# Kernel tuning notes

Hardware: AMD Instinct MI355X
Metric: run time of the kernel (lower is better)

The kernel has to match this reference:

```python
import jax, jax.numpy as jnp
import numpy as np

T, D, TR, CC, L = 4096, 512, 64, 64, 3  # time, input_size, trace, context, num_blocks


def setup_inputs() -> dict:
    key = jax.random.key(0)
    ks = jax.random.split(key, 10)
    x = jax.random.normal(ks[0], (T, D), dtype=jnp.float32)
    state = jnp.zeros((L, 1, TR, CC), dtype=jnp.float32)  # initial recurrent state (real part; imag is 0)
    start = jax.random.uniform(ks[1], (T,)) < 0.02  # episode-reset mask
    Wtr = jax.random.normal(ks[2], (L, TR, D), dtype=jnp.float32) / np.float32(np.sqrt(D))
    Wc = jax.random.normal(ks[3], (L, TR, D), dtype=jnp.float32) / np.float32(np.sqrt(D))
    a = jax.random.uniform(ks[4], (L, TR), minval=1e-6, maxval=0.1)
    b = 2 * jnp.pi / jnp.exp(jax.random.uniform(ks[5], (L, CC), minval=0.0, maxval=float(np.log(10000.0))))
    F = 2 * TR * CC
    W0 = jax.random.normal(ks[6], (L, D, F), dtype=jnp.float32) * np.float32(0.01 / np.sqrt(F))  # default_init scale=0.01
    b0 = jnp.zeros((L, D)); g0 = jnp.ones((L, D)); beta0 = jnp.zeros((L, D))
    W1 = jax.random.normal(ks[7], (L, D, D), dtype=jnp.float32) / np.float32(np.sqrt(D))
    b1 = jnp.zeros((L, D)); g1 = jnp.ones((L, D)); beta1 = jnp.zeros((L, D))
    return dict(x=x, state=state, start=start, Wtr=Wtr, Wc=Wc, a=a, b=b,
                W0=W0, b0=b0, g0=g0, beta0=beta0, W1=W1, b1=b1, g1=g1, beta1=beta1)


def _layernorm(z, g, b):
    m = jnp.mean(z, axis=-1, keepdims=True)
    v = jnp.mean((z - m) ** 2, axis=-1, keepdims=True)
    return (z - m) / jnp.sqrt(v + 1e-5) * g + b


def _sffm(x, st0, start, Wtr, Wc, a, b, W0, b0, g0, bb0, W1, b1, g1, bb1):
    t_len = x.shape[0]
    tr = x @ Wtr.T           # [T, TR]
    ct = x @ Wc.T            # [T, CC] (context proj also has trace_size outputs)
    pre = jnp.abs(tr[:, :, None] * ct[:, None, :])            # [T, TR, CC]
    pre = pre / (1e-8 + jnp.sum(pre, axis=(-2, -1), keepdims=True))
    # complex decay per (trace, context) pair: exp((-|a| + i b) * dt)
    ab = (-jnp.abs(a))[:, None] + 1j * b[None, :]             # [TR, CC] complex64

    def combine(carry, inc):
        ps, s, i = carry
        st, xx, j = inc
        s = s * jnp.logical_not(st)                            # reset gating
        dt = (j - i).astype(jnp.float32)[:, None, None]
        new = s * jnp.exp(ab[None] * dt) + xx
        return (jnp.logical_or(st, ps), new, j)

    ts = jnp.arange(t_len + 1, dtype=jnp.int32)
    sb = jnp.concatenate([jnp.zeros((1, 1, 1), bool), start.reshape(t_len, 1, 1)], axis=0)
    xs = jnp.concatenate([st0.astype(jnp.complex64), pre.astype(jnp.complex64)], axis=0)
    _, ns, _ = jax.lax.associative_scan(combine, (sb, xs, ts), axis=0)
    ns = ns[1:]                                                # [T, TR, CC] complex

    s = ns.reshape(t_len, TR * CC)
    mag = jnp.log1p(jnp.abs(s))
    ang = jnp.angle(s)
    scaled = jnp.concatenate([mag * jnp.sin(ang), mag * jnp.cos(ang)], axis=-1)  # [T, 2*TR*CC]
    z = jax.nn.leaky_relu(_layernorm(scaled @ W0.T + b0, g0, bb0))
    z = jax.nn.leaky_relu(_layernorm(z @ W1.T + b1, g1, bb1))
    return z


def reference(x, state, start, Wtr, Wc, a, b, W0, b0, g0, beta0, W1, b1, g1, beta1):
    z = x
    for l in range(L):
        z = _sffm(x, state[l], start, Wtr[l], Wc[l], a[l], b[l],
                  W0[l], b0[l], g0[l], beta0[l], W1[l], b1[l], g1[l], beta1[l])
        x = x + z
    return z  # NSFFM returns the last block's y
```

## Files before the change

### kernel.cpp

```cpp
#include <hip/hip_runtime.h>
#include <hip/hip_bf16.h>
#include <math.h>

#define T_LEN 4096
#define D_DIM 512
#define F_DIM 8192
#define NCHUNK 64
#define CLEN 64

typedef short short8 __attribute__((ext_vector_type(8)));
typedef float f32x4 __attribute__((ext_vector_type(4)));
typedef unsigned short u16;
typedef unsigned int u32;

__device__ inline float wave_sum(float v) {
#pragma unroll
  for (int o = 32; o; o >>= 1) v += __shfl_xor(v, o);
  return v;
}

__device__ inline u16 f2bf_bits(float v) {
  __hip_bfloat16 h = __float2bfloat16(v);
  return *(u16*)&h;
}

__device__ inline float bf2f(u16 u) {
  u32 x = ((u32)u) << 16;
  return *(float*)&x;
}

__device__ inline void gl_lds16(const void* g, void* l) {
  __builtin_amdgcn_global_load_lds((const __attribute__((address_space(1))) void*)g,
                                   (__attribute__((address_space(3))) void*)l, 16, 0, 0);
}

__global__ void detect_start(const unsigned char* __restrict__ s8, int* __restrict__ mode) {
  __shared__ int found;
  if (threadIdx.x == 0) found = 0;
  __syncthreads();
  for (int i = threadIdx.x; i < 4096; i += 256)
    if ((i & 3) && s8[i]) found = 1;
  __syncthreads();
  if (threadIdx.x == 0) mode[0] = found;
}

__device__ inline int read_start(const unsigned char* s8, const int* s32, int mode, int t) {
  return mode ? (int)s8[t] : s32[t];
}

__global__ void f2bf(const float* __restrict__ s, u16* __restrict__ d, int n) {
  int i = blockIdx.x * 256 + threadIdx.x;
  if (i < n) d[i] = f2bf_bits(s[i]);
}

__global__ void k_conv(const float* __restrict__ wtr, const float* __restrict__ wc,
                       u16* __restrict__ wcat, const float* __restrict__ w0,
                       u16* __restrict__ w0bf) {
  int i = blockIdx.x * 256 + threadIdx.x;
  if (i < 128 * D_DIM) {
    float v = (i < 64 * D_DIM) ? wtr[i] : wc[i - 64 * D_DIM];
    wcat[i] = f2bf_bits(v);
  }
  int j = i - 128 * D_DIM;
  if (j >= 0 && j < D_DIM * F_DIM) {
    int d = j >> 13, f = j & 8191;
    int r = f >> 7, rem = f & 127;
    int c = rem >> 1, b = rem & 1;
    float v = w0[(size_t)d * 8192 + b * 4096 + r * 64 + c];
    w0bf[(size_t)d * 8192 + (f ^ ((d & 7) << 3))] = f2bf_bits(v);
  }
}

template <int BM, int BN, int WR, int WC>
__global__ __launch_bounds__(256) void gemm_bt(const u16* __restrict__ A,
                                               const u16* __restrict__ B,
                                               float* __restrict__ C, int M, int N, int K) {
  constexpr int BK = 32;
  constexpr int MT = BM / (WR * 16);
  constexpr int NT = BN / (WC * 16);
  constexpr int AG = BM / 64;
  constexpr int BG = BN / 64;
  __shared__ u16 sA[BM * BK];
  __shared__ u16 sB[BN * BK];
  const int m0 = blockIdx.x * BM;
  const int n0 = blockIdx.y * BN;
  const int tid = threadIdx.x;
  const int wave = tid >> 6;
  const int lane = tid & 63;
  const int wr = wave / WC;
  const int wc = wave % WC;
  const int row_l = tid >> 2;
  const int c8 = (tid & 3) << 3;
  const int frow = lane & 15;
  const int fcol = (lane >> 4) << 3;

  f32x4 acc[MT][NT];
#pragma unroll
  for (int i = 0; i < MT; ++i)
#pragma unroll
    for (int j = 0; j < NT; ++j) acc[i][j] = (f32x4){0.f, 0.f, 0.f, 0.f};

  for (int k0 = 0; k0 < K; k0 += BK) {
#pragma unroll
    for (int j = 0; j < AG; ++j) {
      uint4 v = *(const uint4*)(A + (size_t)(m0 + j * 64 + row_l) * K + (k0 + c8));
      *(uint4*)(sA + (j * 64 + row_l) * BK + c8) = v;
    }
#pragma unroll
    for (int j = 0; j < BG; ++j) {
      uint4 v = *(const uint4*)(B + (size_t)(n0 + j * 64 + row_l) * K + (k0 + c8));
      *(uint4*)(sB + (j * 64 + row_l) * BK + c8) = v;
    }
    __syncthreads();
    short8 af[MT], bfr[NT];
#pragma unroll
    for (int i = 0; i < MT; ++i)
      af[i] = *(const short8*)(sA + (wr * MT * 16 + i * 16 + frow) * BK + fcol);
#pragma unroll
    for (int j = 0; j < NT; ++j)
      bfr[j] = *(const short8*)(sB + (wc * NT * 16 + j * 16 + frow) * BK + fcol);
#pragma unroll
    for (int i = 0; i < MT; ++i)
#pragma unroll
      for (int j = 0; j < NT; ++j)
        acc[i][j] = __builtin_amdgcn_mfma_f32_16x16x32_bf16(af[i], bfr[j], acc[i][j], 0, 0, 0);
    __syncthreads();
  }
#pragma unroll
  for (int i = 0; i < MT; ++i) {
    const int rbase = m0 + wr * MT * 16 + i * 16 + ((lane >> 4) << 2);
#pragma unroll
    for (int j = 0; j < NT; ++j) {
      const int col = n0 + wc * NT * 16 + j * 16 + (lane & 15);
#pragma unroll
      for (int rg = 0; rg < 4; ++rg) C[(size_t)(rbase + rg) * N + col] = acc[i][j][rg];
    }
  }
}

__global__ __launch_bounds__(256) void gemm128(const u16* __restrict__ A,
                                               const u16* __restrict__ B,
                                               u16* __restrict__ Cp, size_t pstride, int N,
                                               int Ktot) {
  __shared__ u16 sA[128 * 64];
  __shared__ u16 sB[128 * 64];
  const int tid = threadIdx.x;
  const int wave = tid >> 6;
  const int lane = tid & 63;
  const int wr = wave >> 1;
  const int wc = wave & 1;
  const int m0 = blockIdx.x * 128;
  const int n0 = blockIdx.y * 128;
  const int ks = blockIdx.z;
  const int Kper = Ktot / gridDim.z;
  const int kb = ks * Kper;
  const int row_s = tid >> 3;
  const int g8 = (tid & 7) << 3;
  const int frow = lane & 15;
  const int quad = lane >> 4;
  const int sw = frow & 7;

  f32x4 acc[4][4];
#pragma unroll
  for (int i = 0; i < 4; ++i)
#pragma unroll
    for (int j = 0; j < 4; ++j) acc[i][j] = (f32x4){0.f, 0.f, 0.f, 0.f};

  for (int k0 = kb; k0 < kb + Kper; k0 += 64) {
#pragma unroll
    for (int j = 0; j < 4; ++j) {
      gl_lds16(A + (size_t)(m0 + j * 32 + row_s) * Ktot + (k0 + g8), sA + j * 2048 + wave * 512);
      gl_lds16(B + (size_t)(n0 + j * 32 + row_s) * Ktot + (k0 + g8), sB + j * 2048 + wave * 512);
    }
    asm volatile("s_waitcnt vmcnt(0)" ::: "memory");
    __syncthreads();
#pragma unroll
    for (int kk = 0; kk < 2; ++kk) {
      const int gA = (((kk << 2) | quad) ^ sw) << 3;
      short8 af[4], bfr[4];
#pragma unroll
      for (int i = 0; i < 4; ++i)
        af[i] = *(const short8*)(sA + (wr * 64 + i * 16 + frow) * 64 + gA);
#pragma unroll
      for (int j = 0; j < 4; ++j)
        bfr[j] = *(const short8*)(sB + (wc * 64 + j * 16 + frow) * 64 + gA);
#pragma unroll
      for (int i = 0; i < 4; ++i)
#pragma unroll
        for (int j = 0; j < 4; ++j)
          acc[i][j] = __builtin_amdgcn_mfma_f32_16x16x32_bf16(af[i], bfr[j], acc[i][j], 0, 0, 0);
    }
    __syncthreads();
  }
#pragma unroll
  for (int i = 0; i < 4; ++i) {
    const int rbase = m0 + wr * 64 + i * 16 + ((lane >> 4) << 2);
#pragma unroll
    for (int j = 0; j < 4; ++j) {
      const int col = n0 + wc * 64 + j * 16 + (lane & 15);
#pragma unroll
      for (int rg = 0; rg < 4; ++rg)
        Cp[(size_t)ks * pstride + (size_t)(rbase + rg) * N + col] = f2bf_bits(acc[i][j][rg]);
    }
  }
}

__global__ __launch_bounds__(512, 2) void gemm_8ph(const u16* __restrict__ A,
                                                   const u16* __restrict__ B,
                                                   u16* __restrict__ Cp, size_t pstride, int N,
                                                   int Ktot) {
  extern __shared__ u16 smem[];
  u16* sA = smem;
  u16* sB = smem + 32768;
  const int tid = threadIdx.x;
  const int wave = tid >> 6;
  const int lane = tid & 63;
  const int wr = wave >> 1;
  const int wc = wave & 1;
  const int m0 = blockIdx.x * 256;
  const int n0 = blockIdx.y * 128;
  const int ks = blockIdx.z;
  const int Kper = Ktot / gridDim.z;
  const int kb = ks * Kper;
  const int NITER = Kper >> 7;
  const int r_l = tid >> 3;
  const int g8 = (tid & 7) << 3;
  const int frow = lane & 15;
  const int quad = lane >> 4;
  const int sw = frow & 7;

  const u16* Abase = A + (size_t)(m0 + r_l) * Ktot + g8;
  const u16* Bbase = B + (size_t)(n0 + r_l) * Ktot + g8;

#define STAGE_A(l, k0, b) \
  gl_lds16(Abase + (size_t)(l) * 64 * Ktot + (k0), sA + (b)*16384 + (l)*4096 + wave * 512)
#define STAGE_B(l, k0, b) \
  gl_lds16(Bbase + (size_t)(l) * 64 * Ktot + (k0), sB + (b)*8192 + (l)*4096 + wave * 512)

  f32x4 acc[4][4];
#pragma unroll
  for (int i = 0; i < 4; ++i)
#pragma unroll
    for (int j = 0; j < 4; ++j) acc[i][j] = (f32x4){0.f, 0.f, 0.f, 0.f};

  STAGE_A(0, kb, 0);
  STAGE_A(1, kb, 0);
  STAGE_A(2, kb, 0);
  STAGE_A(3, kb, 0);
  STAGE_B(0, kb, 0);
  STAGE_B(1, kb, 0);
  STAGE_A(0, kb + 64, 1);
  STAGE_A(2, kb + 64, 1);
  asm volatile("s_waitcnt vmcnt(2)" ::: "memory");
  __builtin_amdgcn_s_barrier();

  short8 afr[2][2];
  short8 bf0[2][2];
  short8 bf1[2][2];

  for (int I = 0; I < NITER; ++I) {
    const int k0e = kb + (I << 7);
    const bool nl = (I < NITER - 1);
#pragma unroll
    for (int p = 0; p < 8; ++p) {
      const int b = p >> 2;
      const int q = p & 3;
      const int qm = q >> 1;
      const int qn = qm ^ (q & 1);
      if (q == 0 || q == 2) {
#pragma unroll
        for (int f = 0; f < 2; ++f)
#pragma unroll
          for (int kk = 0; kk < 2; ++kk)
            afr[f][kk] = *(const short8*)(sA + b * 16384 +
                                          (wr * 64 + (qm * 2 + f) * 16 + frow) * 64 +
                                          ((((kk << 2) | quad) ^ sw) << 3));
      }
      if (q == 0) {
#pragma unroll
        for (int g = 0; g < 2; ++g)
#pragma unroll
          for (int kk = 0; kk < 2; ++kk)
            bf0[g][kk] = *(const short8*)(sB + b * 8192 + (wc * 64 + g * 16 + frow) * 64 +
                                          ((((kk << 2) | quad) ^ sw) << 3));
      }
      if (q == 1) {
#pragma unroll
        for (int g = 0; g < 2; ++g)
#pragma unroll
          for (int kk = 0; kk < 2; ++kk)
            bf1[g][kk] = *(const short8*)(sB + b * 8192 + (wc * 64 + 32 + g * 16 + frow) * 64 +
                                          ((((kk << 2) | quad) ^ sw) << 3));
      }
      if (p == 0) { STAGE_A(1, k0e + 64, 1); STAGE_A(3, k0e + 64, 1); }
      if (p == 1) { STAGE_B(0, k0e + 64, 1); STAGE_B(1, k0e + 64, 1); }
      if (p == 3 && nl) { STAGE_A(0, k0e + 128, 0); STAGE_A(2, k0e + 128, 0); }
      if (p == 4 && nl) { STAGE_A(1, k0e + 128, 0); STAGE_A(3, k0e + 128, 0); }
      if (p == 5 && nl) { STAGE_B(0, k0e + 128, 0); STAGE_B(1, k0e + 128, 0); }
      if (p == 7 && nl) { STAGE_A(0, k0e + 192, 1); STAGE_A(2, k0e + 192, 1); }
      __builtin_amdgcn_s_barrier();
      asm volatile("s_waitcnt lgkmcnt(0)" ::: "memory");
      __builtin_amdgcn_sched_barrier(0);
      __builtin_amdgcn_s_setprio(1);
      if (qn == 0) {
#pragma unroll
        for (int f = 0; f < 2; ++f)
#pragma unroll
          for (int g = 0; g < 2; ++g)
#pragma unroll
            for (int kk = 0; kk < 2; ++kk)
              acc[qm * 2 + f][g] = __builtin_amdgcn_mfma_f32_16x16x32_bf16(
                  afr[f][kk], bf0[g][kk], acc[qm * 2 + f][g], 0, 0, 0);
      } else {
#pragma unroll
        for (int f = 0; f < 2; ++f)
#pragma unroll
          for (int g = 0; g < 2; ++g)
#pragma unroll
            for (int kk = 0; kk < 2; ++kk)
              acc[qm * 2 + f][2 + g] = __builtin_amdgcn_mfma_f32_16x16x32_bf16(
                  afr[f][kk], bf1[g][kk], acc[qm * 2 + f][2 + g], 0, 0, 0);
      }
      __builtin_amdgcn_s_setprio(0);
      if (p == 3) {
        if (nl)
          asm volatile("s_waitcnt vmcnt(2)" ::: "memory");
        else
          asm volatile("s_waitcnt vmcnt(0)" ::: "memory");
      }
      if (p == 7 && nl) asm volatile("s_waitcnt vmcnt(2)" ::: "memory");
      __builtin_amdgcn_s_barrier();
    }
  }
#undef STAGE_A
#undef STAGE_B

#pragma unroll
  for (int i = 0; i < 4; ++i) {
    const int rbase = m0 + wr * 64 + i * 16 + (quad << 2);
#pragma unroll
    for (int j = 0; j < 4; ++j) {
      const int col = n0 + wc * 64 + j * 16 + frow;
#pragma unroll
      for (int rg = 0; rg < 4; ++rg)
        Cp[(size_t)ks * pstride + (size_t)(rbase + rg) * N + col] = f2bf_bits(acc[i][j][rg]);
    }
  }
}

__global__ void prep_pq(const float* __restrict__ trct, float* __restrict__ pT,
                        float* __restrict__ q) {
  int t = blockIdx.x;
  int lane = threadIdx.x;
  float tr = trct[t * 128 + lane];
  float ct = trct[t * 128 + 64 + lane];
  float ap = fabsf(tr), aq = fabsf(ct);
  float Sp = wave_sum(ap);
  float Sq = wave_sum(aq);
  float denom = 1e-8f + Sp * Sq;
  pT[lane * T_LEN + t] = ap;
  q[t * 64 + lane] = aq / denom;
}

__global__ void scan_phase1(const float* __restrict__ pT, const float* __restrict__ q,
                            const unsigned char* __restrict__ st8, const int* __restrict__ st32,
                            const int* __restrict__ modep, const float* __restrict__ a,
                            const float* __restrict__ b, float4* __restrict__ chunkbuf) {
  int chunk = blockIdx.x, r = blockIdx.y, c = threadIdx.x;
  int mode = modep[0];
  int t0 = chunk * CLEN;
  float na = -fabsf(a[r]);
  float rho = __expf(na);
  float bb = b[c];
  float er = rho * __cosf(bb), ei = rho * __sinf(bb);
  float pv = pT[r * T_LEN + t0 + c];
  int sv = read_start(st8, st32, mode, t0 + c);
  unsigned long long bal = __ballot(sv != 0);
  float Ar, Ai;
  if (bal) {
    Ar = 0.f; Ai = 0.f;
  } else {
    float mag = __expf(64.f * na);
    float ang = 64.f * bb;
    Ar = mag * __cosf(ang);
    Ai = mag * __sinf(ang);
  }
  int L = bal ? (63 - __builtin_clzll(bal)) : 0;
  float Br = 0.f, Bi = 0.f;
  const float* qrow = q + (size_t)t0 * 64 + c;
  for (int i = L; i < CLEN; ++i) {
    float pre = __shfl(pv, i) * qrow[i * 64];
    float nBr = er * Br - ei * Bi + pre;
    Bi = er * Bi + ei * Br;
    Br = nBr;
  }
  chunkbuf[((size_t)chunk * 64 + r) * 64 + c] = make_float4(Ar, Ai, Br, Bi);
}

__global__ void scan_phase2(const float4* __restrict__ chunkbuf, const float* __restrict__ state,
                            float2* __restrict__ s0buf) {
  int r = blockIdx.x, c = threadIdx.x;
  float Sr = state[r * 64 + c], Si = 0.f;
  for (int k = 0; k < NCHUNK; ++k) {
    s0buf[((size_t)k * 64 + r) * 64 + c] = make_float2(Sr, Si);
    float4 ab = chunkbuf[((size_t)k * 64 + r) * 64 + c];
    float nSr = ab.x * Sr - ab.y * Si + ab.z;
    Si = ab.x * Si + ab.y * Sr + ab.w;
    Sr = nSr;
  }
}

__global__ void scan_phase3(const float* __restrict__ pT, const float* __restrict__ q,
                            const unsigned char* __restrict__ st8, const int* __restrict__ st32,
                            const int* __restrict__ modep, const float* __restrict__ a,
                            const float* __restrict__ b, const float2* __restrict__ s0buf,
                            u32* __restrict__ scaled, int c0) {
  int chunk = c0 + blockIdx.x, r = blockIdx.y, c = threadIdx.x;
  int mode = modep[0];
  int t0 = chunk * CLEN;
  float rho = __expf(-fabsf(a[r]));
  float bb = b[c];
  float er = rho * __cosf(bb), ei = rho * __sinf(bb);
  float pv = pT[r * T_LEN + t0 + c];
  int sv = read_start(st8, st32, mode, t0 + c);
  float2 s0 = s0buf[((size_t)chunk * 64 + r) * 64 + c];
  float Sr = s0.x, Si = s0.y;
  int tl0 = (chunk - c0) * CLEN;
  const float* qrow = q + (size_t)t0 * 64 + c;
  u32* srow = scaled + (size_t)tl0 * 4096;
  const int Ldw = r * 64 + c;
#pragma unroll 4
  for (int i = 0; i < CLEN; ++i) {
    float qt = qrow[i * 64];
    float pt = __shfl(pv, i);
    int st = __shfl(sv, i);
    float pre = pt * qt;
    float cer = st ? 0.f : er;
    float cei = st ? 0.f : ei;
    float nSr = cer * Sr - cei * Si + pre;
    Si = cer * Si + cei * Sr;
    Sr = nSr;
    float m2 = fmaf(Sr, Sr, Si * Si);
    float rsq = rsqrtf(fmaxf(m2, 1e-30f));
    float m = m2 * rsq;
    float sc = __log2f(1.0f + m) * 0.6931471805599453f * rsq;
    u32 pack = ((u32)f2bf_bits(sc * Sr) << 16) | (u32)f2bf_bits(sc * Si);
    srow[(size_t)i * 4096 + (Ldw ^ ((i & 7) << 2))] = pack;
  }
}

__global__ void ln_act16(const u16* __restrict__ parts, int KS, size_t pstride,
                         const float* __restrict__ bias, const float* __restrict__ gam,
                         const float* __restrict__ bet, u16* __restrict__ zbf) {
  __shared__ float red[8];
  int t = blockIdx.x, tid = threadIdx.x;
  size_t o = (size_t)t * D_DIM + tid;
  float v0 = bias[tid];
  float v1 = bias[tid + 256];
  for (int ks = 0; ks < KS; ++ks) {
    v0 += bf2f(parts[(size_t)ks * pstride + o]);
    v1 += bf2f(parts[(size_t)ks * pstride + o + 256]);
  }
  float s = wave_sum(v0 + v1);
  if ((tid & 63) == 0) red[tid >> 6] = s;
  __syncthreads();
  float mean = (red[0] + red[1] + red[2] + red[3]) * (1.f / 512.f);
  float d0 = v0 - mean, d1 = v1 - mean;
  float s2 = wave_sum(d0 * d0 + d1 * d1);
  if ((tid & 63) == 0) red[4 + (tid >> 6)] = s2;
  __syncthreads();
  float var = (red[4] + red[5] + red[6] + red[7]) * (1.f / 512.f);
  float rstd = rsqrtf(var + 1e-5f);
  float z0 = d0 * rstd * gam[tid] + bet[tid];
  float z1 = d1 * rstd * gam[tid + 256] + bet[tid + 256];
  z0 = z0 > 0.f ? z0 : 0.01f * z0;
  z1 = z1 > 0.f ? z1 : 0.01f * z1;
  zbf[o] = f2bf_bits(z0);
  zbf[o + 256] = f2bf_bits(z1);
}

__global__ void ln_act32(const float* __restrict__ y, const float* __restrict__ bias,
                         const float* __restrict__ gam, const float* __restrict__ bet,
                         const float* __restrict__ xsrc, float* __restrict__ xdst,
                         u16* __restrict__ xbf_next, float* __restrict__ finout) {
  __shared__ float red[8];
  int t = blockIdx.x, tid = threadIdx.x;
  size_t o = (size_t)t * D_DIM + tid;
  float v0 = y[o] + bias[tid];
  float v1 = y[o + 256] + bias[tid + 256];
  float s = wave_sum(v0 + v1);
  if ((tid & 63) == 0) red[tid >> 6] = s;
  __syncthreads();
  float mean = (red[0] + red[1] + red[2] + red[3]) * (1.f / 512.f);
  float d0 = v0 - mean, d1 = v1 - mean;
  float s2 = wave_sum(d0 * d0 + d1 * d1);
  if ((tid & 63) == 0) red[4 + (tid >> 6)] = s2;
  __syncthreads();
  float var = (red[4] + red[5] + red[6] + red[7]) * (1.f / 512.f);
  float rstd = rsqrtf(var + 1e-5f);
  float z0 = d0 * rstd * gam[tid] + bet[tid];
  float z1 = d1 * rstd * gam[tid + 256] + bet[tid + 256];
  z0 = z0 > 0.f ? z0 : 0.01f * z0;
  z1 = z1 > 0.f ? z1 : 0.01f * z1;
  if (xdst) {
    float x0 = xsrc[o] + z0, x1 = xsrc[o + 256] + z1;
    xdst[o] = x0;
    xdst[o + 256] = x1;
    xbf_next[o] = f2bf_bits(x0);
    xbf_next[o + 256] = f2bf_bits(x1);
  }
  if (finout) {
    finout[o] = z0;
    finout[o + 256] = z1;
  }
}

__global__ void err_signal(float* __restrict__ out, float code) {
  if (threadIdx.x == 0) out[0] = code;
}

extern "C" void kernel_launch(void* const* d_in, const int* in_sizes, int n_in, void* d_out,
                              int out_size, void* d_ws, size_t ws_size, hipStream_t stream) {
  const float* x_in = (const float*)d_in[0];
  const float* state = (const float*)d_in[1];
  const unsigned char* start8 = (const unsigned char*)d_in[2];
  const int* start32 = (const int*)d_in[2];
  const float* Wtr = (const float*)d_in[3];
  const float* Wc = (const float*)d_in[4];
  const float* a_in = (const float*)d_in[5];
  const float* b_in = (const float*)d_in[6];
  const float* W0 = (const float*)d_in[7];
  const float* b0 = (const float*)d_in[8];
  const float* g0 = (const float*)d_in[9];
  const float* beta0 = (const float*)d_in[10];
  const float* W1 = (const float*)d_in[11];
  const float* b1 = (const float*)d_in[12];
  const float* g1 = (const float*)d_in[13];
  const float* beta1 = (const float*)d_in[14];
  float* out = (float*)d_out;

  static int attr_state = 0;
  if (attr_state == 0)
    attr_state = (hipFuncSetAttribute((const void*)gemm_8ph,
                                      hipFuncAttributeMaxDynamicSharedMemorySize,
                                      98304) == hipSuccess)
                     ? 1
                     : -1;
  const bool attr_ok = (attr_state == 1);

  char* w = (char*)d_ws;
  auto alloc = [&](size_t bytes) {
    char* ptr = w;
    w += (bytes + 255) & ~(size_t)255;
    return ptr;
  };
  float* x_ws = (float*)alloc(4ull * T_LEN * D_DIM);
  u16* xbf = (u16*)alloc(2ull * T_LEN * D_DIM);
  u16* wcat = (u16*)alloc(2ull * 128 * D_DIM);
  u16* w0bf = (u16*)alloc(2ull * D_DIM * F_DIM);
  u16* w1bf = (u16*)alloc(2ull * 3 * D_DIM * D_DIM);
  float* trct = (float*)alloc(4ull * T_LEN * 128);
  float* pTbuf = (float*)alloc(4ull * T_LEN * 64);
  float* qbuf = (float*)alloc(4ull * T_LEN * 64);
  float4* chunkbuf = (float4*)alloc(16ull * NCHUNK * 64 * 64);
  float2* s0buf = (float2*)alloc(8ull * NCHUNK * 64 * 64);
  u16* z0bf = (u16*)alloc(2ull * T_LEN * D_DIM);
  float* ybuf = (float*)alloc(4ull * T_LEN * D_DIM);
  int* modep = (int*)alloc(256);
  size_t base1 = (size_t)(w - (char*)d_ws);

  if (n_in != 15) {
    err_signal<<<1, 64, 0, stream>>>(out, 9e6f + 1000.f * n_in);
    return;
  }
  const size_t MB = 1ull << 20;
  const size_t pstride = (size_t)T_LEN * D_DIM;
  int KS, nseg;
  if (ws_size >= base1 + 16 * MB + 64 * MB) { KS = 4; nseg = 1; }
  else if (ws_size >= base1 + 16 * MB + 32 * MB) { KS = 4; nseg = 2; }
  else if (ws_size >= base1 + 8 * MB + 32 * MB) { KS = 2; nseg = 2; }
  else if (ws_size >= base1 + 8 * MB + 16 * MB) { KS = 2; nseg = 4; }
  else if (ws_size >= base1 + 4 * MB + 16 * MB) { KS = 1; nseg = 4; }
  else {
    err_signal<<<1, 64, 0, stream>>>(out, 9e6f);
    return;
  }
  const int seg_rows = T_LEN / nseg;
  const int seg_chunks = NCHUNK / nseg;
  u16* ypart = (u16*)alloc(2ull * KS * pstride);
  u16* scaled = (u16*)alloc(2ull * seg_rows * F_DIM);

  const bool use8 = (nseg == 1) && attr_ok;

  detect_start<<<1, 256, 0, stream>>>(start8, modep);
  f2bf<<<(T_LEN * D_DIM) / 256, 256, 0, stream>>>(x_in, xbf, T_LEN * D_DIM);
  f2bf<<<(3 * D_DIM * D_DIM) / 256, 256, 0, stream>>>(W1, w1bf, 3 * D_DIM * D_DIM);

  for (int l = 0; l < 3; ++l) {
    const float* Wtr_l = Wtr + (size_t)l * 64 * D_DIM;
    const float* Wc_l = Wc + (size_t)l * 64 * D_DIM;
    const float* a_l = a_in + l * 64;
    const float* b_l = b_in + l * 64;
    const float* W0_l = W0 + (size_t)l * D_DIM * F_DIM;
    const u16* w1bf_l = w1bf + (size_t)l * D_DIM * D_DIM;
    const float* state_l = state + (size_t)l * 64 * 64;
    const float* xsrc = (l == 0) ? x_in : x_ws;

    k_conv<<<(128 * D_DIM + D_DIM * F_DIM) / 256, 256, 0, stream>>>(Wtr_l, Wc_l, wcat, W0_l,
                                                                    w0bf);
    gemm_bt<64, 64, 2, 2><<<dim3(T_LEN / 64, 2), 256, 0, stream>>>(xbf, wcat, trct, T_LEN, 128,
                                                                   D_DIM);
    prep_pq<<<T_LEN, 64, 0, stream>>>(trct, pTbuf, qbuf);
    scan_phase1<<<dim3(NCHUNK, 64), 64, 0, stream>>>(pTbuf, qbuf, start8, start32, modep, a_l,
                                                     b_l, chunkbuf);
    scan_phase2<<<64, 64, 0, stream>>>(chunkbuf, state_l, s0buf);

    for (int h = 0; h < nseg; ++h) {
      scan_phase3<<<dim3(seg_chunks, 64), 64, 0, stream>>>(pTbuf, qbuf, start8, start32, modep,
                                                           a_l, b_l, s0buf, (u32*)scaled,
                                                           h * seg_chunks);
      if (use8)
        gemm_8ph<<<dim3(seg_rows / 256, D_DIM / 128, KS), 512, 98304, stream>>>(
            scaled, w0bf, ypart + (size_t)h * seg_rows * D_DIM, pstride, D_DIM, F_DIM);
      else
        gemm128<<<dim3(seg_rows / 128, D_DIM / 128, KS), 256, 0, stream>>>(
            scaled, w0bf, ypart + (size_t)h * seg_rows * D_DIM, pstride, D_DIM, F_DIM);
    }
    ln_act16<<<T_LEN, 256, 0, stream>>>(ypart, KS, pstride, b0 + l * D_DIM, g0 + l * D_DIM,
                                        beta0 + l * D_DIM, z0bf);
    gemm_bt<64, 64, 2, 2><<<dim3(T_LEN / 64, D_DIM / 64), 256, 0, stream>>>(z0bf, w1bf_l, ybuf,
                                                                            T_LEN, D_DIM, D_DIM);
    ln_act32<<<T_LEN, 256, 0, stream>>>(ybuf, b1 + l * D_DIM, g1 + l * D_DIM, beta1 + l * D_DIM,
                                        (l < 2) ? xsrc : nullptr, (l < 2) ? x_ws : nullptr,
                                        (l < 2) ? xbf : nullptr, (l == 2) ? out : nullptr);
  }
}
```

Baseline: 495.7 us.

## Software-pipeline LDS fragment reads one phase ahead of MFMA in GEMM

Restructures the bf16 GEMM main loop so shared-memory fragment loads for the next phase are issued before the current phase's MFMAs. Partial lgkmcnt waits replace full drains, and the global-to-LDS staging schedule and vmcnt waits are reshuffled to fit. The aim is to hide LDS read latency behind matrix math. It adds register pressure from extra fragment buffers and makes the barrier/waitcnt ordering fragile, with a risk of races.

```diff
diff --git a/kernel.cpp b/kernel.cpp
--- a/kernel.cpp
+++ b/kernel.cpp
@@ -228,6 +228,8 @@
   const int frow = lane & 15;
   const int quad = lane >> 4;
   const int sw = frow & 7;
+  const int o0 = (quad ^ sw) << 3;
+  const int o1 = ((4 | quad) ^ sw) << 3;
 
   const u16* Abase = A + (size_t)(m0 + r_l) * Ktot + g8;
   const u16* Bbase = B + (size_t)(n0 + r_l) * Ktot + g8;
@@ -236,12 +238,34 @@
   gl_lds16(Abase + (size_t)(l) * 64 * Ktot + (k0), sA + (b)*16384 + (l)*4096 + wave * 512)
 #define STAGE_B(l, k0, b) \
   gl_lds16(Bbase + (size_t)(l) * 64 * Ktot + (k0), sB + (b)*8192 + (l)*4096 + wave * 512)
+#define RD_A(dst, b, qm_)                                                          \
+  do {                                                                             \
+    const u16* _p = sA + (b)*16384 + (wr * 64 + (qm_)*32 + frow) * 64;             \
+    dst[0][0] = *(const short8*)(_p + o0);                                         \
+    dst[0][1] = *(const short8*)(_p + o1);                                         \
+    dst[1][0] = *(const short8*)(_p + 1024 + o0);                                  \
+    dst[1][1] = *(const short8*)(_p + 1024 + o1);                                  \
+  } while (0)
+#define RD_B(dst, b, half_)                                                        \
+  do {                                                                             \
+    const u16* _p = sB + (b)*8192 + (wc * 64 + (half_)*32 + frow) * 64;            \
+    dst[0][0] = *(const short8*)(_p + o0);                                         \
+    dst[0][1] = *(const short8*)(_p + o1);                                         \
+    dst[1][0] = *(const short8*)(_p + 1024 + o0);                                  \
+    dst[1][1] = *(const short8*)(_p + 1024 + o1);                                  \
+  } while (0)
 
   f32x4 acc[4][4];
 #pragma unroll
   for (int i = 0; i < 4; ++i)
 #pragma unroll
     for (int j = 0; j < 4; ++j) acc[i][j] = (f32x4){0.f, 0.f, 0.f, 0.f};
+
+  short8 af_lo[2][2];
+  short8 af_hi[2][2];
+  short8 bf1r[2][2];
+  short8 bf0A[2][2];
+  short8 bf0B[2][2];
 
   STAGE_A(0, kb, 0);
   STAGE_A(1, kb, 0);
@@ -251,89 +275,91 @@
   STAGE_B(1, kb, 0);
   STAGE_A(0, kb + 64, 1);
   STAGE_A(2, kb + 64, 1);
-  asm volatile("s_waitcnt vmcnt(2)" ::: "memory");
+  STAGE_A(1, kb + 64, 1);
+  STAGE_A(3, kb + 64, 1);
+  asm volatile("s_waitcnt vmcnt(4)" ::: "memory");
   __builtin_amdgcn_s_barrier();
-
-  short8 afr[2][2];
-  short8 bf0[2][2];
-  short8 bf1[2][2];
+  RD_A(af_lo, 0, 0);
+  RD_B(bf0A, 0, 0);
 
   for (int I = 0; I < NITER; ++I) {
     const int k0e = kb + (I << 7);
     const bool nl = (I < NITER - 1);
 #pragma unroll
     for (int p = 0; p < 8; ++p) {
-      const int b = p >> 2;
-      const int q = p & 3;
-      const int qm = q >> 1;
-      const int qn = qm ^ (q & 1);
-      if (q == 0 || q == 2) {
-#pragma unroll
-        for (int f = 0; f < 2; ++f)
-#pragma unroll
-          for (int kk = 0; kk < 2; ++kk)
-            afr[f][kk] = *(const short8*)(sA + b * 16384 +
-                                          (wr * 64 + (qm * 2 + f) * 16 + frow) * 64 +
-                                          ((((kk << 2) | quad) ^ sw) << 3));
+      if (p == 0) RD_B(bf1r, 0, 1);
+      if (p == 1) RD_A(af_hi, 0, 1);
+      if (p == 2) RD_A(af_lo, 1, 0);
+      if (p == 3) RD_B(bf0B, 1, 0);
+      if (p == 4) RD_B(bf1r, 1, 1);
+      if (p == 5) RD_A(af_hi, 1, 1);
+      if (p == 6 && nl) RD_A(af_lo, 0, 0);
+      if (p == 7 && nl) RD_B(bf0A, 0, 0);
+      __builtin_amdgcn_s_barrier();
+      if (p == 6 || p == 7) {
+        if (nl)
+          asm volatile("s_waitcnt lgkmcnt(4)" ::: "memory");
+        else
+          asm volatile("s_waitcnt lgkmcnt(0)" ::: "memory");
+      } else {
+        asm volatile("s_waitcnt lgkmcnt(4)" ::: "memory");
       }
-      if (q == 0) {
+      __builtin_amdgcn_sched_barrier(0);
+      if (p == 0) { STAGE_B(0, k0e + 64, 1); STAGE_B(1, k0e + 64, 1); }
+      if (p == 2 && nl) { STAGE_A(0, k0e + 128, 0); STAGE_A(2, k0e + 128, 0); }
+      if (p == 3 && nl) { STAGE_A(1, k0e + 128, 0); STAGE_A(3, k0e + 128, 0); }
+      if (p == 4 && nl) { STAGE_B(0, k0e + 128, 0); STAGE_B(1, k0e + 128, 0); }
+      if (p == 6 && nl) { STAGE_A(0, k0e + 192, 1); STAGE_A(2, k0e + 192, 1); }
+      if (p == 7 && nl) { STAGE_A(1, k0e + 192, 1); STAGE_A(3, k0e + 192, 1); }
+      __builtin_amdgcn_s_setprio(1);
+#pragma unroll
+      for (int f = 0; f < 2; ++f)
 #pragma unroll
         for (int g = 0; g < 2; ++g)
 #pragma unroll
-          for (int kk = 0; kk < 2; ++kk)
-            bf0[g][kk] = *(const short8*)(sB + b * 8192 + (wc * 64 + g * 16 + frow) * 64 +
-                                          ((((kk << 2) | quad) ^ sw) << 3));
-      }
-      if (q == 1) {
-#pragma unroll
-        for (int g = 0; g < 2; ++g)
-#pragma unroll
-          for (int kk = 0; kk < 2; ++kk)
-            bf1[g][kk] = *(const short8*)(sB + b * 8192 + (wc * 64 + 32 + g * 16 + frow) * 64 +
-                                          ((((kk << 2) | quad) ^ sw) << 3));
-      }
-      if (p == 0) { STAGE_A(1, k0e + 64, 1); STAGE_A(3, k0e + 64, 1); }
-      if (p == 1) { STAGE_B(0, k0e + 64, 1); STAGE_B(1, k0e + 64, 1); }
-      if (p == 3 && nl) { STAGE_A(0, k0e + 128, 0); STAGE_A(2, k0e + 128, 0); }
-      if (p == 4 && nl) { STAGE_A(1, k0e + 128, 0); STAGE_A(3, k0e + 128, 0); }
-      if (p == 5 && nl) { STAGE_B(0, k0e + 128, 0); STAGE_B(1, k0e + 128, 0); }
-      if (p == 7 && nl) { STAGE_A(0, k0e + 192, 1); STAGE_A(2, k0e + 192, 1); }
-      __builtin_amdgcn_s_barrier();
-      asm volatile("s_waitcnt lgkmcnt(0)" ::: "memory");
-      __builtin_amdgcn_sched_barrier(0);
-      __builtin_amdgcn_s_setprio(1);
-      if (qn == 0) {
-#pragma unroll
-        for (int f = 0; f < 2; ++f)
-#pragma unroll
-          for (int g = 0; g < 2; ++g)
-#pragma unroll
-            for (int kk = 0; kk < 2; ++kk)
-              acc[qm * 2 + f][g] = __builtin_amdgcn_mfma_f32_16x16x32_bf16(
-                  afr[f][kk], bf0[g][kk], acc[qm * 2 + f][g], 0, 0, 0);
-      } else {
-#pragma unroll
-        for (int f = 0; f < 2; ++f)
-#pragma unroll
-          for (int g = 0; g < 2; ++g)
-#pragma unroll
-            for (int kk = 0; kk < 2; ++kk)
-              acc[qm * 2 + f][2 + g] = __builtin_amdgcn_mfma_f32_16x16x32_bf16(
-                  afr[f][kk], bf1[g][kk], acc[qm * 2 + f][2 + g], 0, 0, 0);
-      }
+          for (int kk = 0; kk < 2; ++kk) {
+            if (p == 0)
+              acc[f][g] = __builtin_amdgcn_mfma_f32_16x16x32_bf16(af_lo[f][kk], bf0A[g][kk],
+                                                                  acc[f][g], 0, 0, 0);
+            if (p == 1)
+              acc[f][2 + g] = __builtin_amdgcn_mfma_f32_16x16x32_bf16(af_lo[f][kk], bf1r[g][kk],
+                                                                      acc[f][2 + g], 0, 0, 0);
+            if (p == 2)
+              acc[2 + f][2 + g] = __builtin_amdgcn_mfma_f32_16x16x32_bf16(
+                  af_hi[f][kk], bf1r[g][kk], acc[2 + f][2 + g], 0, 0, 0);
+            if (p == 3)
+              acc[2 + f][g] = __builtin_amdgcn_mfma_f32_16x16x32_bf16(af_hi[f][kk], bf0A[g][kk],
+                                                                      acc[2 + f][g], 0, 0, 0);
+            if (p == 4)
+              acc[f][g] = __builtin_amdgcn_mfma_f32_16x16x32_bf16(af_lo[f][kk], bf0B[g][kk],
+                                                                  acc[f][g], 0, 0, 0);
+            if (p == 5)
+              acc[f][2 + g] = __builtin_amdgcn_mfma_f32_16x16x32_bf16(af_lo[f][kk], bf1r[g][kk],
+                                                                      acc[f][2 + g], 0, 0, 0);
+            if (p == 6)
+              acc[2 + f][2 + g] = __builtin_amdgcn_mfma_f32_16x16x32_bf16(
+                  af_hi[f][kk], bf1r[g][kk], acc[2 + f][2 + g], 0, 0, 0);
+            if (p == 7)
+              acc[2 + f][g] = __builtin_amdgcn_mfma_f32_16x16x32_bf16(af_hi[f][kk], bf0B[g][kk],
+                                                                      acc[2 + f][g], 0, 0, 0);
+          }
       __builtin_amdgcn_s_setprio(0);
-      if (p == 3) {
+      if (p == 1) asm volatile("s_waitcnt vmcnt(2)" ::: "memory");
+      if (p == 2) {
         if (nl)
           asm volatile("s_waitcnt vmcnt(2)" ::: "memory");
         else
           asm volatile("s_waitcnt vmcnt(0)" ::: "memory");
       }
-      if (p == 7 && nl) asm volatile("s_waitcnt vmcnt(2)" ::: "memory");
+      if (p == 5 && nl) asm volatile("s_waitcnt vmcnt(2)" ::: "memory");
+      if (p == 6 && nl) asm volatile("s_waitcnt vmcnt(2)" ::: "memory");
       __builtin_amdgcn_s_barrier();
     }
   }
 #undef STAGE_A
 #undef STAGE_B
+#undef RD_A
+#undef RD_B
 
 #pragma unroll
   for (int i = 0; i < 4; ++i) {
```

Measured after the change: 495.0 us. Within noise of the previous version (-0.1%).

## Restructure GEMM main loop into 4 phases with whole-tile prefetch

Applied to the files above, without the earlier changes.

Replaces the 8-phase per-iteration pipeline, which interleaved small global-to-LDS stages, with four larger phases. B fragments are loaded once per half-tile and reused across both A halves, which cuts LDS reads. All six stage loads for the next buffer are issued at once, followed by full vmcnt(0) waits. This removes barriers and LDS traffic, but the coarser waits can expose more global-load latency.

```diff
diff --git a/kernel.cpp b/kernel.cpp
--- a/kernel.cpp
+++ b/kernel.cpp
@@ -228,6 +228,8 @@
   const int frow = lane & 15;
   const int quad = lane >> 4;
   const int sw = frow & 7;
+  const int o0 = (quad ^ sw) << 3;
+  const int o1 = ((4 | quad) ^ sw) << 3;
 
   const u16* Abase = A + (size_t)(m0 + r_l) * Ktot + g8;
   const u16* Bbase = B + (size_t)(n0 + r_l) * Ktot + g8;
@@ -236,12 +238,49 @@
   gl_lds16(Abase + (size_t)(l) * 64 * Ktot + (k0), sA + (b)*16384 + (l)*4096 + wave * 512)
 #define STAGE_B(l, k0, b) \
   gl_lds16(Bbase + (size_t)(l) * 64 * Ktot + (k0), sB + (b)*8192 + (l)*4096 + wave * 512)
+#define RD_A(dst, b, qm_)                                               \
+  do {                                                                  \
+    const u16* _p = sA + (b)*16384 + (wr * 64 + (qm_)*32 + frow) * 64;  \
+    dst[0][0] = *(const short8*)(_p + o0);                              \
+    dst[0][1] = *(const short8*)(_p + o1);                              \
+    dst[1][0] = *(const short8*)(_p + 1024 + o0);                       \
+    dst[1][1] = *(const short8*)(_p + 1024 + o1);                       \
+  } while (0)
+#define RD_B(dst, b, half_)                                              \
+  do {                                                                   \
+    const u16* _p = sB + (b)*8192 + (wc * 64 + (half_)*32 + frow) * 64;  \
+    dst[0][0] = *(const short8*)(_p + o0);                               \
+    dst[0][1] = *(const short8*)(_p + o1);                               \
+    dst[1][0] = *(const short8*)(_p + 1024 + o0);                        \
+    dst[1][1] = *(const short8*)(_p + 1024 + o1);                        \
+  } while (0)
+#define MFMA_QPAIR(ar, b0_, b1_, qm_)                                               \
+  do {                                                                              \
+    _Pragma("unroll") for (int f = 0; f < 2; ++f) _Pragma("unroll") for (int g = 0; \
+                                                                         g < 2;    \
+                                                                         ++g)      \
+        _Pragma("unroll") for (int kk = 0; kk < 2; ++kk) acc[(qm_)*2 + f][g] =      \
+            __builtin_amdgcn_mfma_f32_16x16x32_bf16(ar[f][kk], b0_[g][kk],          \
+                                                    acc[(qm_)*2 + f][g], 0, 0, 0); \
+    _Pragma("unroll") for (int f = 0; f < 2; ++f) _Pragma("unroll") for (int g = 0; \
+                                                                         g < 2;    \
+                                                                         ++g)      \
+        _Pragma("unroll") for (int kk = 0; kk < 2; ++kk) acc[(qm_)*2 + f][2 + g] =  \
+            __builtin_amdgcn_mfma_f32_16x16x32_bf16(ar[f][kk], b1_[g][kk],          \
+                                                    acc[(qm_)*2 + f][2 + g], 0, 0,  \
+                                                    0);                             \
+  } while (0)
 
   f32x4 acc[4][4];
 #pragma unroll
   for (int i = 0; i < 4; ++i)
 #pragma unroll
     for (int j = 0; j < 4; ++j) acc[i][j] = (f32x4){0.f, 0.f, 0.f, 0.f};
+
+  short8 af_lo[2][2];
+  short8 af_hi[2][2];
+  short8 bfr0[2][2];
+  short8 bfr1[2][2];
 
   STAGE_A(0, kb, 0);
   STAGE_A(1, kb, 0);
@@ -249,91 +288,104 @@
   STAGE_A(3, kb, 0);
   STAGE_B(0, kb, 0);
   STAGE_B(1, kb, 0);
-  STAGE_A(0, kb + 64, 1);
-  STAGE_A(2, kb + 64, 1);
-  asm volatile("s_waitcnt vmcnt(2)" ::: "memory");
+  asm volatile("s_waitcnt vmcnt(0)" ::: "memory");
   __builtin_amdgcn_s_barrier();
-
-  short8 afr[2][2];
-  short8 bf0[2][2];
-  short8 bf1[2][2];
 
   for (int I = 0; I < NITER; ++I) {
     const int k0e = kb + (I << 7);
     const bool nl = (I < NITER - 1);
-#pragma unroll
-    for (int p = 0; p < 8; ++p) {
-      const int b = p >> 2;
-      const int q = p & 3;
-      const int qm = q >> 1;
-      const int qn = qm ^ (q & 1);
-      if (q == 0 || q == 2) {
-#pragma unroll
-        for (int f = 0; f < 2; ++f)
-#pragma unroll
-          for (int kk = 0; kk < 2; ++kk)
-            afr[f][kk] = *(const short8*)(sA + b * 16384 +
-                                          (wr * 64 + (qm * 2 + f) * 16 + frow) * 64 +
-                                          ((((kk << 2) | quad) ^ sw) << 3));
-      }
-      if (q == 0) {
-#pragma unroll
-        for (int g = 0; g < 2; ++g)
-#pragma unroll
-          for (int kk = 0; kk < 2; ++kk)
-            bf0[g][kk] = *(const short8*)(sB + b * 8192 + (wc * 64 + g * 16 + frow) * 64 +
-                                          ((((kk << 2) | quad) ^ sw) << 3));
-      }
-      if (q == 1) {
-#pragma unroll
-        for (int g = 0; g < 2; ++g)
-#pragma unroll
-          for (int kk = 0; kk < 2; ++kk)
-            bf1[g][kk] = *(const short8*)(sB + b * 8192 + (wc * 64 + 32 + g * 16 + frow) * 64 +
-                                          ((((kk << 2) | quad) ^ sw) << 3));
-      }
-      if (p == 0) { STAGE_A(1, k0e + 64, 1); STAGE_A(3, k0e + 64, 1); }
-      if (p == 1) { STAGE_B(0, k0e + 64, 1); STAGE_B(1, k0e + 64, 1); }
-      if (p == 3 && nl) { STAGE_A(0, k0e + 128, 0); STAGE_A(2, k0e + 128, 0); }
-      if (p == 4 && nl) { STAGE_A(1, k0e + 128, 0); STAGE_A(3, k0e + 128, 0); }
-      if (p == 5 && nl) { STAGE_B(0, k0e + 128, 0); STAGE_B(1, k0e + 128, 0); }
-      if (p == 7 && nl) { STAGE_A(0, k0e + 192, 1); STAGE_A(2, k0e + 192, 1); }
-      __builtin_amdgcn_s_barrier();
-      asm volatile("s_waitcnt lgkmcnt(0)" ::: "memory");
-      __builtin_amdgcn_sched_barrier(0);
-      __builtin_amdgcn_s_setprio(1);
-      if (qn == 0) {
-#pragma unroll
-        for (int f = 0; f < 2; ++f)
-#pragma unroll
-          for (int g = 0; g < 2; ++g)
-#pragma unroll
-            for (int kk = 0; kk < 2; ++kk)
-              acc[qm * 2 + f][g] = __builtin_amdgcn_mfma_f32_16x16x32_bf16(
-                  afr[f][kk], bf0[g][kk], acc[qm * 2 + f][g], 0, 0, 0);
-      } else {
-#pragma unroll
-        for (int f = 0; f < 2; ++f)
-#pragma unroll
-          for (int g = 0; g < 2; ++g)
-#pragma unroll
-            for (int kk = 0; kk < 2; ++kk)
-              acc[qm * 2 + f][2 + g] = __builtin_amdgcn_mfma_f32_16x16x32_bf16(
-                  afr[f][kk], bf1[g][kk], acc[qm * 2 + f][2 + g], 0, 0, 0);
-      }
-      __builtin_amdgcn_s_setprio(0);
-      if (p == 3) {
-        if (nl)
-          asm volatile("s_waitcnt vmcnt(2)" ::: "memory");
-        else
-          asm volatile("s_waitcnt vmcnt(0)" ::: "memory");
-      }
-      if (p == 7 && nl) asm volatile("s_waitcnt vmcnt(2)" ::: "memory");
-      __builtin_amdgcn_s_barrier();
-    }
+
+    RD_A(af_lo, 0, 0);
+    RD_B(bfr0, 0, 0);
+    RD_B(bfr1, 0, 1);
+    STAGE_A(0, k0e + 64, 1);
+    STAGE_A(1, k0e + 64, 1);
+    STAGE_A(2, k0e + 64, 1);
+    STAGE_A(3, k0e + 64, 1);
+    STAGE_B(0, k0e + 64, 1);
+    STAGE_B(1, k0e + 64, 1);
+    __builtin_amdgcn_s_barrier();
+    asm volatile("s_waitcnt lgkmcnt(0)" ::: "memory");
+    __builtin_amdgcn_sched_barrier(0);
+    __builtin_amdgcn_s_setprio(1);
+    MFMA_QPAIR(af_lo, bfr0, bfr1, 0);
+    __builtin_amdgcn_s_setprio(0);
+    __builtin_amdgcn_s_barrier();
+
+    RD_A(af_hi, 0, 1);
+    __builtin_amdgcn_s_barrier();
+    asm volatile("s_waitcnt lgkmcnt(0)" ::: "memory");
+    __builtin_amdgcn_sched_barrier(0);
+    __builtin_amdgcn_s_setprio(1);
+#pragma unroll
+    for (int f = 0; f < 2; ++f)
+#pragma unroll
+      for (int g = 0; g < 2; ++g)
+#pragma unroll
+        for (int kk = 0; kk < 2; ++kk)
+          acc[2 + f][2 + g] = __builtin_amdgcn_mfma_f32_16x16x32_bf16(
+              af_hi[f][kk], bfr1[g][kk], acc[2 + f][2 + g], 0, 0, 0);
+#pragma unroll
+    for (int f = 0; f < 2; ++f)
+#pragma unroll
+      for (int g = 0; g < 2; ++g)
+#pragma unroll
+        for (int kk = 0; kk < 2; ++kk)
+          acc[2 + f][g] = __builtin_amdgcn_mfma_f32_16x16x32_bf16(af_hi[f][kk], bfr0[g][kk],
+                                                                  acc[2 + f][g], 0, 0, 0);
+    __builtin_amdgcn_s_setprio(0);
+    asm volatile("s_waitcnt vmcnt(0)" ::: "memory");
+    __builtin_amdgcn_s_barrier();
+
+    RD_A(af_lo, 1, 0);
+    RD_B(bfr0, 1, 0);
+    RD_B(bfr1, 1, 1);
+    if (nl) {
+      STAGE_A(0, k0e + 128, 0);
+      STAGE_A(1, k0e + 128, 0);
+      STAGE_A(2, k0e + 128, 0);
+      STAGE_A(3, k0e + 128, 0);
+      STAGE_B(0, k0e + 128, 0);
+      STAGE_B(1, k0e + 128, 0);
+    }
+    __builtin_amdgcn_s_barrier();
+    asm volatile("s_waitcnt lgkmcnt(0)" ::: "memory");
+    __builtin_amdgcn_sched_barrier(0);
+    __builtin_amdgcn_s_setprio(1);
+    MFMA_QPAIR(af_lo, bfr0, bfr1, 0);
+    __builtin_amdgcn_s_setprio(0);
+    __builtin_amdgcn_s_barrier();
+
+    RD_A(af_hi, 1, 1);
+    __builtin_amdgcn_s_barrier();
+    asm volatile("s_waitcnt lgkmcnt(0)" ::: "memory");
+    __builtin_amdgcn_sched_barrier(0);
+    __builtin_amdgcn_s_setprio(1);
+#pragma unroll
+    for (int f = 0; f < 2; ++f)
+#pragma unroll
+      for (int g = 0; g < 2; ++g)
+#pragma unroll
+        for (int kk = 0; kk < 2; ++kk)
+          acc[2 + f][2 + g] = __builtin_amdgcn_mfma_f32_16x16x32_bf16(
+              af_hi[f][kk], bfr1[g][kk], acc[2 + f][2 + g], 0, 0, 0);
+#pragma unroll
+    for (int f = 0; f < 2; ++f)
+#pragma unroll
+      for (int g = 0; g < 2; ++g)
+#pragma unroll
+        for (int kk = 0; kk < 2; ++kk)
+          acc[2 + f][g] = __builtin_amdgcn_mfma_f32_16x16x32_bf16(af_hi[f][kk], bfr0[g][kk],
+                                                                  acc[2 + f][g], 0, 0, 0);
+    __builtin_amdgcn_s_setprio(0);
+    if (nl) asm volatile("s_waitcnt vmcnt(0)" ::: "memory");
+    __builtin_amdgcn_s_barrier();
   }
 #undef STAGE_A
 #undef STAGE_B
+#undef RD_A
+#undef RD_B
+#undef MFMA_QPAIR
 
 #pragma unroll
   for (int i = 0; i < 4; ++i) {
```

Result: no change. 495.9 us (+0.1%).

## Load B fragments directly from global and triple-buffer A in LDS

Applied to the files above, without the earlier changes.

The 8-phase GEMM main loop is rewritten. B tiles now skip LDS and go straight from global memory into registers, while A tiles get a three-deep LDS ring with one barrier per 64-wide K step. All 32 MFMAs for a step are issued together after a single wait. This removes LDS traffic and barriers for B, but exposes global-load latency for B inside each iteration, since B is loaded and consumed in the same step.

```diff
diff --git a/kernel.cpp b/kernel.cpp
--- a/kernel.cpp
+++ b/kernel.cpp
@@ -211,7 +211,6 @@
                                                    int Ktot) {
   extern __shared__ u16 smem[];
   u16* sA = smem;
-  u16* sB = smem + 32768;
   const int tid = threadIdx.x;
   const int wave = tid >> 6;
   const int lane = tid & 63;
@@ -222,118 +221,123 @@
   const int ks = blockIdx.z;
   const int Kper = Ktot / gridDim.z;
   const int kb = ks * Kper;
-  const int NITER = Kper >> 7;
+  const int nT = Kper >> 6;
   const int r_l = tid >> 3;
   const int g8 = (tid & 7) << 3;
   const int frow = lane & 15;
   const int quad = lane >> 4;
   const int sw = frow & 7;
+  const int o0 = (quad ^ sw) << 3;
+  const int o1 = ((4 | quad) ^ sw) << 3;
 
   const u16* Abase = A + (size_t)(m0 + r_l) * Ktot + g8;
-  const u16* Bbase = B + (size_t)(n0 + r_l) * Ktot + g8;
+  const u16* Bbase = B + (size_t)(n0 + wc * 64 + frow) * (size_t)Ktot;
 
 #define STAGE_A(l, k0, b) \
   gl_lds16(Abase + (size_t)(l) * 64 * Ktot + (k0), sA + (b)*16384 + (l)*4096 + wave * 512)
-#define STAGE_B(l, k0, b) \
-  gl_lds16(Bbase + (size_t)(l) * 64 * Ktot + (k0), sB + (b)*8192 + (l)*4096 + wave * 512)
+#define RD_A(dst, b, qm_)                                               \
+  do {                                                                  \
+    const u16* _p = sA + (b)*16384 + (wr * 64 + (qm_)*32 + frow) * 64;  \
+    dst[0][0] = *(const short8*)(_p + o0);                              \
+    dst[0][1] = *(const short8*)(_p + o1);                              \
+    dst[1][0] = *(const short8*)(_p + 1024 + o0);                       \
+    dst[1][1] = *(const short8*)(_p + 1024 + o1);                       \
+  } while (0)
+#define GLB_B(dst, half_)                                          \
+  do {                                                             \
+    const u16* _q = Bk + (size_t)((half_)*32) * Ktot;              \
+    dst[0][0] = *(const short8*)(_q + o0);                         \
+    dst[0][1] = *(const short8*)(_q + o1);                         \
+    dst[1][0] = *(const short8*)(_q + (size_t)16 * Ktot + o0);     \
+    dst[1][1] = *(const short8*)(_q + (size_t)16 * Ktot + o1);     \
+  } while (0)
 
   f32x4 acc[4][4];
 #pragma unroll
   for (int i = 0; i < 4; ++i)
 #pragma unroll
     for (int j = 0; j < 4; ++j) acc[i][j] = (f32x4){0.f, 0.f, 0.f, 0.f};
+
+  short8 af_lo[2][2];
+  short8 af_hi[2][2];
+  short8 bfr0[2][2];
+  short8 bfr1[2][2];
 
   STAGE_A(0, kb, 0);
   STAGE_A(1, kb, 0);
   STAGE_A(2, kb, 0);
   STAGE_A(3, kb, 0);
-  STAGE_B(0, kb, 0);
-  STAGE_B(1, kb, 0);
   STAGE_A(0, kb + 64, 1);
+  STAGE_A(1, kb + 64, 1);
   STAGE_A(2, kb + 64, 1);
-  asm volatile("s_waitcnt vmcnt(2)" ::: "memory");
+  STAGE_A(3, kb + 64, 1);
+  asm volatile("s_waitcnt vmcnt(4)" ::: "memory");
   __builtin_amdgcn_s_barrier();
 
-  short8 afr[2][2];
-  short8 bf0[2][2];
-  short8 bf1[2][2];
-
-  for (int I = 0; I < NITER; ++I) {
-    const int k0e = kb + (I << 7);
-    const bool nl = (I < NITER - 1);
-#pragma unroll
-    for (int p = 0; p < 8; ++p) {
-      const int b = p >> 2;
-      const int q = p & 3;
-      const int qm = q >> 1;
-      const int qn = qm ^ (q & 1);
-      if (q == 0 || q == 2) {
-#pragma unroll
-        for (int f = 0; f < 2; ++f)
-#pragma unroll
-          for (int kk = 0; kk < 2; ++kk)
-            afr[f][kk] = *(const short8*)(sA + b * 16384 +
-                                          (wr * 64 + (qm * 2 + f) * 16 + frow) * 64 +
-                                          ((((kk << 2) | quad) ^ sw) << 3));
-      }
-      if (q == 0) {
-#pragma unroll
-        for (int g = 0; g < 2; ++g)
-#pragma unroll
-          for (int kk = 0; kk < 2; ++kk)
-            bf0[g][kk] = *(const short8*)(sB + b * 8192 + (wc * 64 + g * 16 + frow) * 64 +
-                                          ((((kk << 2) | quad) ^ sw) << 3));
-      }
-      if (q == 1) {
-#pragma unroll
-        for (int g = 0; g < 2; ++g)
-#pragma unroll
-          for (int kk = 0; kk < 2; ++kk)
-            bf1[g][kk] = *(const short8*)(sB + b * 8192 + (wc * 64 + 32 + g * 16 + frow) * 64 +
-                                          ((((kk << 2) | quad) ^ sw) << 3));
-      }
-      if (p == 0) { STAGE_A(1, k0e + 64, 1); STAGE_A(3, k0e + 64, 1); }
-      if (p == 1) { STAGE_B(0, k0e + 64, 1); STAGE_B(1, k0e + 64, 1); }
-      if (p == 3 && nl) { STAGE_A(0, k0e + 128, 0); STAGE_A(2, k0e + 128, 0); }
-      if (p == 4 && nl) { STAGE_A(1, k0e + 128, 0); STAGE_A(3, k0e + 128, 0); }
-      if (p == 5 && nl) { STAGE_B(0, k0e + 128, 0); STAGE_B(1, k0e + 128, 0); }
-      if (p == 7 && nl) { STAGE_A(0, k0e + 192, 1); STAGE_A(2, k0e + 192, 1); }
-      __builtin_amdgcn_s_barrier();
-      asm volatile("s_waitcnt lgkmcnt(0)" ::: "memory");
-      __builtin_amdgcn_sched_barrier(0);
-      __builtin_amdgcn_s_setprio(1);
-      if (qn == 0) {
-#pragma unroll
-        for (int f = 0; f < 2; ++f)
-#pragma unroll
-          for (int g = 0; g < 2; ++g)
-#pragma unroll
-            for (int kk = 0; kk < 2; ++kk)
-              acc[qm * 2 + f][g] = __builtin_amdgcn_mfma_f32_16x16x32_bf16(
-                  afr[f][kk], bf0[g][kk], acc[qm * 2 + f][g], 0, 0, 0);
-      } else {
-#pragma unroll
-        for (int f = 0; f < 2; ++f)
-#pragma unroll
-          for (int g = 0; g < 2; ++g)
-#pragma unroll
-            for (int kk = 0; kk < 2; ++kk)
-              acc[qm * 2 + f][2 + g] = __builtin_amdgcn_mfma_f32_16x16x32_bf16(
-                  afr[f][kk], bf1[g][kk], acc[qm * 2 + f][2 + g], 0, 0, 0);
-      }
-      __builtin_amdgcn_s_setprio(0);
-      if (p == 3) {
-        if (nl)
-          asm volatile("s_waitcnt vmcnt(2)" ::: "memory");
-        else
-          asm volatile("s_waitcnt vmcnt(0)" ::: "memory");
-      }
-      if (p == 7 && nl) asm volatile("s_waitcnt vmcnt(2)" ::: "memory");
-      __builtin_amdgcn_s_barrier();
-    }
+  int bc = 0;
+  for (int t = 0; t < nT; ++t) {
+    const int k0 = kb + (t << 6);
+    int bs = bc + 2;
+    if (bs >= 3) bs -= 3;
+    const bool nl = (t + 2 < nT);
+    const u16* Bk = Bbase + k0;
+    GLB_B(bfr0, 0);
+    GLB_B(bfr1, 1);
+    RD_A(af_lo, bc, 0);
+    RD_A(af_hi, bc, 1);
+    if (nl) {
+      STAGE_A(0, k0 + 128, bs);
+      STAGE_A(1, k0 + 128, bs);
+      STAGE_A(2, k0 + 128, bs);
+      STAGE_A(3, k0 + 128, bs);
+    }
+    if (nl)
+      asm volatile("s_waitcnt vmcnt(4)" ::: "memory");
+    else
+      asm volatile("s_waitcnt vmcnt(0)" ::: "memory");
+    asm volatile("s_waitcnt lgkmcnt(0)" ::: "memory");
+    __builtin_amdgcn_sched_barrier(0);
+    __builtin_amdgcn_s_setprio(1);
+#pragma unroll
+    for (int f = 0; f < 2; ++f)
+#pragma unroll
+      for (int g = 0; g < 2; ++g)
+#pragma unroll
+        for (int kk = 0; kk < 2; ++kk)
+          acc[f][g] = __builtin_amdgcn_mfma_f32_16x16x32_bf16(af_lo[f][kk], bfr0[g][kk],
+                                                              acc[f][g], 0, 0, 0);
+#pragma unroll
+    for (int f = 0; f < 2; ++f)
+#pragma unroll
+      for (int g = 0; g < 2; ++g)
+#pragma unroll
+        for (int kk = 0; kk < 2; ++kk)
+          acc[f][2 + g] = __builtin_amdgcn_mfma_f32_16x16x32_bf16(af_lo[f][kk], bfr1[g][kk],
+                                                                  acc[f][2 + g], 0, 0, 0);
+#pragma unroll
+    for (int f = 0; f < 2; ++f)
+#pragma unroll
+      for (int g = 0; g < 2; ++g)
+#pragma unroll
+        for (int kk = 0; kk < 2; ++kk)
+          acc[2 + f][2 + g] = __builtin_amdgcn_mfma_f32_16x16x32_bf16(
+              af_hi[f][kk], bfr1[g][kk], acc[2 + f][2 + g], 0, 0, 0);
+#pragma unroll
+    for (int f = 0; f < 2; ++f)
+#pragma unroll
+      for (int g = 0; g < 2; ++g)
+#pragma unroll
+        for (int kk = 0; kk < 2; ++kk)
+          acc[2 + f][g] = __builtin_amdgcn_mfma_f32_16x16x32_bf16(af_hi[f][kk], bfr0[g][kk],
+                                                                  acc[2 + f][g], 0, 0, 0);
+    __builtin_amdgcn_s_setprio(0);
+    __builtin_amdgcn_s_barrier();
+    bc += 1;
+    if (bc >= 3) bc -= 3;
   }
 #undef STAGE_A
-#undef STAGE_B
+#undef RD_A
+#undef GLB_B
 
 #pragma unroll
   for (int i = 0; i < 4; ++i) {
```

Result: slower. 563.5 us (+13.7%).
